# Optimization experiments

Hardware: AMD Instinct MI355X
Metric: run time of the kernel (lower is better)

Reference implementation:

```python
import jax, jax.numpy as jnp
import numpy as np

B, N, D, E, R = 2, 50000, 128, 500000, 500
LN_EPS = 1e-5


def setup_inputs() -> dict:
    key = jax.random.key(0)
    ks = jax.random.split(key, 12)
    s = 1.0 / np.sqrt(D)
    s2 = 1.0 / np.sqrt(2 * D)
    return {
        "h": jax.random.normal(ks[0], (B, N, D), dtype=jnp.float32),
        "edge_src": jax.random.randint(ks[1], (E,), 0, N),
        "edge_tgt": jax.random.randint(ks[2], (E,), 0, N),
        "edge_rel": jax.random.randint(ks[3], (E,), 0, R),
        "nE": N,
        "msg_W": jax.random.uniform(ks[4], (D, D), jnp.float32, -s, s),
        "rel_emb": jax.random.normal(ks[5], (R, D), dtype=jnp.float32),
        "gate_W": jax.random.uniform(ks[6], (D, D), jnp.float32, -s, s),
        "update_W": jax.random.uniform(ks[7], (2 * D, D), jnp.float32, -s2, s2),
        "update_b": jax.random.uniform(ks[8], (D,), jnp.float32, -s2, s2),
        "ln_gamma": jnp.ones((D,), jnp.float32),
        "ln_beta": jnp.zeros((D,), jnp.float32),
    }


def reference(h, edge_src, edge_tgt, edge_rel, nE, msg_W, rel_emb, gate_W,
              update_W, update_b, ln_gamma, ln_beta):
    r = rel_emb[edge_rel]                      # [E, D]
    h_src = h[:, edge_src]                     # [B, E, D] gather
    gate = jax.nn.sigmoid(h_src @ gate_W)      # [B, E, D]
    msg = (h_src @ msg_W) * r[None] * gate     # [B, E, D]
    # scatter_add over target nodes
    h_agg = jnp.zeros((h.shape[0], nE, h.shape[2]), h.dtype)
    h_agg = h_agg.at[:, edge_tgt].add(msg)     # [B, N, D]
    upd = jnp.concatenate([h, h_agg], axis=-1) @ update_W + update_b
    x = h + jax.nn.relu(upd)
    mu = jnp.mean(x, axis=-1, keepdims=True)
    var = jnp.var(x, axis=-1, keepdims=True)
    h_new = (x - mu) * jax.lax.rsqrt(var + LN_EPS) * ln_gamma + ln_beta
    return h_new
```

## Files before the change

### kernel.cpp

```cpp
#include <hip/hip_runtime.h>

#define DD 128
#define NN 50000
#define BB 2
#define EE 500000
#define CAP 64
#define LN_EPS 1e-5f

typedef __attribute__((ext_vector_type(8))) short bf16x8;
typedef __attribute__((ext_vector_type(4))) float f32x4;

union FragU { unsigned short u[8]; unsigned int q[4]; bf16x8 v; };

__device__ __forceinline__ unsigned short f2bf(float x) {
  union { float f; unsigned u; } v; v.f = x;
  unsigned r = (v.u + 0x7FFFu + ((v.u >> 16) & 1u)) >> 16;
  return (unsigned short)r;
}
__device__ __forceinline__ float bfbits(short s) {
  union { unsigned u; float f; } v;
  v.u = ((unsigned)(unsigned short)s) << 16;
  return v.f;
}
__device__ __forceinline__ float sigmoidf(float x) {
  return 1.0f / (1.0f + __expf(-x));
}

__device__ __forceinline__ void stage16(const void* g, void* l) {
  __builtin_amdgcn_global_load_lds(
      (const __attribute__((address_space(1))) unsigned int*)g,
      (__attribute__((address_space(3))) unsigned int*)l, 16, 0, 0);
}

__global__ __launch_bounds__(256) void k_node(
    const float* __restrict__ h, const float* __restrict__ gate_W,
    const float* __restrict__ msg_W, unsigned short* __restrict__ P,
    int* __restrict__ deg, int BN)
{
  __shared__ float Hs[3][2048];

  const int t    = threadIdx.x;

  {
    const int gid  = blockIdx.x * 256 + t;
    const int gsz2 = gridDim.x * 256;
    for (int i = gid; i < NN; i += gsz2) deg[i] = 0;
    asm volatile("s_waitcnt vmcnt(0)" ::: "memory");
    __builtin_amdgcn_sched_barrier(0);
  }

  const int lane = t & 63;
  const int n16  = lane & 15;
  const int quad = lane >> 4;
  const int wave = t >> 6;

  FragU ag[2][4], am[2][4];
#pragma unroll
  for (int fi = 0; fi < 2; fi++) {
    const int frow = (wave + fi * 4) * 16 + n16;
#pragma unroll
    for (int ks = 0; ks < 4; ks++) {
      const int k0 = ks * 32 + quad * 8;
#pragma unroll
      for (int e = 0; e < 8; e++) {
        ag[fi][ks].u[e] = f2bf(gate_W[(size_t)(k0 + e) * DD + frow]);
        am[fi][ks].u[e] = f2bf(msg_W[(size_t)(k0 + e) * DD + frow]);
      }
    }
  }

  const int sr = t >> 5, sc = t & 31;
  const size_t g0 = (size_t)sr * 512 +
                    (size_t)((((sc & 24) | ((sc & 7) ^ (sr & 7)))) << 4);

  const int nT    = BN >> 4;
  const int gstep = gridDim.x;
  const int bid   = blockIdx.x;
  const char* hB  = (const char*)h;

#define NSTAGE(slot, tl)                                                     \
  do {                                                                       \
    const char* gb = hB + ((size_t)(tl) << 13);                              \
    char* lb = (char*)&Hs[slot][0];                                          \
    stage16(gb + g0, lb + t * 16);                                           \
    stage16(gb + g0 + 4096, lb + 4096 + t * 16);                             \
  } while (0)

  if (bid < nT)         NSTAGE(0, bid);
  if (bid + gstep < nT) NSTAGE(1, bid + gstep);

  int s = 0;
  for (int tile = bid; tile < nT; tile += gstep) {
    asm volatile("s_waitcnt vmcnt(2)" ::: "memory");
    __builtin_amdgcn_s_barrier();
    asm volatile("" ::: "memory");
    __builtin_amdgcn_sched_barrier(0);

    const float* hs = &Hs[s][0];
    bf16x8 bfr[4];
#pragma unroll
    for (int ks = 0; ks < 4; ks++) {
      const int cc = ks * 8 + quad * 2;
      const int w0 = (cc & 24) | ((cc & 7) ^ (n16 & 7));
      const int w1 = ((cc + 1) & 24) | (((cc + 1) & 7) ^ (n16 & 7));
      const float4 x0 = *(const float4*)(hs + n16 * 128 + w0 * 4);
      const float4 x1 = *(const float4*)(hs + n16 * 128 + w1 * 4);
      FragU f;
      f.u[0] = f2bf(x0.x); f.u[1] = f2bf(x0.y);
      f.u[2] = f2bf(x0.z); f.u[3] = f2bf(x0.w);
      f.u[4] = f2bf(x1.x); f.u[5] = f2bf(x1.y);
      f.u[6] = f2bf(x1.z); f.u[7] = f2bf(x1.w);
      bfr[ks] = f.v;
    }

    f32x4 accg[2], accm[2];
#pragma unroll
    for (int fi = 0; fi < 2; fi++) { accg[fi] = (f32x4)0.f; accm[fi] = (f32x4)0.f; }

#pragma unroll
    for (int fi = 0; fi < 2; fi++)
#pragma unroll
      for (int ks = 0; ks < 4; ks++) {
        accg[fi] = __builtin_amdgcn_mfma_f32_16x16x32_bf16(ag[fi][ks].v, bfr[ks], accg[fi], 0, 0, 0);
        accm[fi] = __builtin_amdgcn_mfma_f32_16x16x32_bf16(am[fi][ks].v, bfr[ks], accm[fi], 0, 0, 0);
      }

    const int b    = (tile * 16 >= NN) ? 1 : 0;
    const int node = tile * 16 + n16 - b * NN;
    unsigned short* Pr = P + (size_t)node * 256 + b * 128;
#pragma unroll
    for (int fi = 0; fi < 2; fi++) {
      const int ft = wave + fi * 4;
      const float v0 = accm[fi][0] * sigmoidf(accg[fi][0]);
      const float v1 = accm[fi][1] * sigmoidf(accg[fi][1]);
      const float v2 = accm[fi][2] * sigmoidf(accg[fi][2]);
      const float v3 = accm[fi][3] * sigmoidf(accg[fi][3]);
      uint2 o;
      o.x = (unsigned int)f2bf(v0) | ((unsigned int)f2bf(v1) << 16);
      o.y = (unsigned int)f2bf(v2) | ((unsigned int)f2bf(v3) << 16);
      *(uint2*)(Pr + ft * 16 + quad * 4) = o;
    }

    asm volatile("" ::: "memory");
    if (tile + 2 * gstep < nT) {
      int s2 = s + 2; if (s2 >= 3) s2 -= 3;
      NSTAGE(s2, tile + 2 * gstep);
    }
    s = (s + 1 >= 3) ? 0 : s + 1;
  }
#undef NSTAGE
}

__global__ __launch_bounds__(256) void k_fill_direct(
    const int* __restrict__ esrc, const int* __restrict__ etgt,
    const int* __restrict__ erel, int* __restrict__ deg,
    int* __restrict__ packed)
{
  const int e = blockIdx.x * 256 + threadIdx.x;
  if (e < EE) {
    const int tgt = etgt[e];
    const int pos = atomicAdd(&deg[tgt], 1);
    if (pos < CAP) packed[(size_t)tgt * CAP + pos] = esrc[e] | (erel[e] << 16);
  }
}

__global__ __launch_bounds__(256) void k_agg(
    const unsigned short* __restrict__ P, const float* __restrict__ rel_emb,
    const int* __restrict__ deg, const int* __restrict__ packed,
    unsigned short* __restrict__ h_agg)
{
  const int node = blockIdx.x * 4 + (threadIdx.x >> 6);
  if (node >= NN) return;
  const int lane = threadIdx.x & 63;
  const int half = lane >> 5;
  const int c8   = (lane & 31) * 8;
  const int rc   = c8 & 127;

  const int beg = node * CAP;
  const int cnt = min(deg[node], CAP);
  const int end = beg + cnt;

  float acc[8];
#pragma unroll
  for (int i = 0; i < 8; i++) acc[i] = 0.f;

  int j = beg + half;
  for (; j + 2 < end; j += 4) {
    const int p0 = packed[j];
    const int p1 = packed[j + 2];
    const bf16x8 pv0 = *(const bf16x8*)(P + (size_t)(p0 & 0xFFFF) * 256 + c8);
    const float4 ra0 = *(const float4*)(rel_emb + (size_t)(p0 >> 16) * DD + rc);
    const float4 rb0 = *(const float4*)(rel_emb + (size_t)(p0 >> 16) * DD + rc + 4);
    const bf16x8 pv1 = *(const bf16x8*)(P + (size_t)(p1 & 0xFFFF) * 256 + c8);
    const float4 ra1 = *(const float4*)(rel_emb + (size_t)(p1 >> 16) * DD + rc);
    const float4 rb1 = *(const float4*)(rel_emb + (size_t)(p1 >> 16) * DD + rc + 4);
    acc[0] += bfbits(pv0[0]) * ra0.x;  acc[0] += bfbits(pv1[0]) * ra1.x;
    acc[1] += bfbits(pv0[1]) * ra0.y;  acc[1] += bfbits(pv1[1]) * ra1.y;
    acc[2] += bfbits(pv0[2]) * ra0.z;  acc[2] += bfbits(pv1[2]) * ra1.z;
    acc[3] += bfbits(pv0[3]) * ra0.w;  acc[3] += bfbits(pv1[3]) * ra1.w;
    acc[4] += bfbits(pv0[4]) * rb0.x;  acc[4] += bfbits(pv1[4]) * rb1.x;
    acc[5] += bfbits(pv0[5]) * rb0.y;  acc[5] += bfbits(pv1[5]) * rb1.y;
    acc[6] += bfbits(pv0[6]) * rb0.z;  acc[6] += bfbits(pv1[6]) * rb1.z;
    acc[7] += bfbits(pv0[7]) * rb0.w;  acc[7] += bfbits(pv1[7]) * rb1.w;
  }
  for (; j < end; j += 2) {
    const int p0 = packed[j];
    const bf16x8 pv0 = *(const bf16x8*)(P + (size_t)(p0 & 0xFFFF) * 256 + c8);
    const float4 ra0 = *(const float4*)(rel_emb + (size_t)(p0 >> 16) * DD + rc);
    const float4 rb0 = *(const float4*)(rel_emb + (size_t)(p0 >> 16) * DD + rc + 4);
    acc[0] += bfbits(pv0[0]) * ra0.x;
    acc[1] += bfbits(pv0[1]) * ra0.y;
    acc[2] += bfbits(pv0[2]) * ra0.z;
    acc[3] += bfbits(pv0[3]) * ra0.w;
    acc[4] += bfbits(pv0[4]) * rb0.x;
    acc[5] += bfbits(pv0[5]) * rb0.y;
    acc[6] += bfbits(pv0[6]) * rb0.z;
    acc[7] += bfbits(pv0[7]) * rb0.w;
  }

#pragma unroll
  for (int i = 0; i < 8; i++) acc[i] += __shfl_xor(acc[i], 32, 64);

  if (half == 0) {
    uint4 o;
    o.x = (unsigned int)f2bf(acc[0]) | ((unsigned int)f2bf(acc[1]) << 16);
    o.y = (unsigned int)f2bf(acc[2]) | ((unsigned int)f2bf(acc[3]) << 16);
    o.z = (unsigned int)f2bf(acc[4]) | ((unsigned int)f2bf(acc[5]) << 16);
    o.w = (unsigned int)f2bf(acc[6]) | ((unsigned int)f2bf(acc[7]) << 16);
    *(uint4*)(h_agg + (size_t)node * 256 + c8) = o;
  }
}

__global__ __launch_bounds__(256) void k_update_ln(
    const float* __restrict__ h, const unsigned short* __restrict__ h_agg,
    const float* __restrict__ upd_W, const float* __restrict__ upd_b,
    const float* __restrict__ gamma, const float* __restrict__ beta,
    float* __restrict__ out, int BN)
{
  __shared__ float Us[3][3072];
  __shared__ float Rs[4][16], Rq[4][16];

  const int t    = threadIdx.x;
  const int lane = t & 63;
  const int n16  = lane & 15;
  const int quad = lane >> 4;
  const int wave = t >> 6;

  FragU aw[2][8];
#pragma unroll
  for (int fi = 0; fi < 2; fi++) {
    const int frow = (wave + fi * 4) * 16 + n16;
#pragma unroll
    for (int ks = 0; ks < 8; ks++) {
      const int k0 = ks * 32 + quad * 8;
#pragma unroll
      for (int e = 0; e < 8; e++)
        aw[fi][ks].u[e] = f2bf(upd_W[(size_t)(k0 + e) * DD + frow]);
    }
  }

  float4 bv[2], gv[2], btv[2];
#pragma unroll
  for (int fi = 0; fi < 2; fi++) {
    const int f0 = (wave + fi * 4) * 16 + quad * 4;
    bv[fi]  = *(const float4*)(upd_b + f0);
    gv[fi]  = *(const float4*)(gamma + f0);
    btv[fi] = *(const float4*)(beta + f0);
  }

  const int sr = t >> 5, sc = t & 31;
  const size_t g0 = (size_t)sr * 512 +
                    (size_t)((((sc & 24) | ((sc & 7) ^ (sr & 7)))) << 4);
  const int ar = t >> 4, ac = t & 15;
  const size_t ga0 = (size_t)ar * 512 +
                     (size_t)((((ac & 8) | ((ac & 7) ^ (ar & 7)))) << 4);

  const int nT    = BN >> 4;
  const int gstep = gridDim.x;
  const int bid   = blockIdx.x;
  const char* hB  = (const char*)h;
  const char* aB  = (const char*)h_agg;

#define USTAGE(slot, tl)                                                     \
  do {                                                                       \
    const char* gb = hB + ((size_t)(tl) << 13);                              \
    char* lb = (char*)&Us[slot][0];                                          \
    stage16(gb + g0, lb + t * 16);                                           \
    stage16(gb + g0 + 4096, lb + 4096 + t * 16);                             \
    const int bb = ((tl) * 16 >= NN) ? 1 : 0;                                \
    const size_t node0 = (size_t)(tl) * 16 - (size_t)bb * NN;                \
    stage16(aB + (node0 << 9) + ((size_t)bb << 8) + ga0, lb + 8192 + t * 16);\
  } while (0)

  if (bid < nT)         USTAGE(0, bid);
  if (bid + gstep < nT) USTAGE(1, bid + gstep);

  int s = 0;
  for (int tile = bid; tile < nT; tile += gstep) {
    asm volatile("s_waitcnt vmcnt(3)" ::: "memory");
    __builtin_amdgcn_s_barrier();
    asm volatile("" ::: "memory");
    __builtin_amdgcn_sched_barrier(0);

    const float* hs = &Us[s][0];
    const unsigned short* ha = (const unsigned short*)(hs + 2048);

    bf16x8 bfr[8];
#pragma unroll
    for (int ks = 0; ks < 4; ks++) {
      const int cc = ks * 8 + quad * 2;
      const int w0 = (cc & 24) | ((cc & 7) ^ (n16 & 7));
      const int w1 = ((cc + 1) & 24) | (((cc + 1) & 7) ^ (n16 & 7));
      const float4 x0 = *(const float4*)(hs + n16 * 128 + w0 * 4);
      const float4 x1 = *(const float4*)(hs + n16 * 128 + w1 * 4);
      FragU f;
      f.u[0] = f2bf(x0.x); f.u[1] = f2bf(x0.y);
      f.u[2] = f2bf(x0.z); f.u[3] = f2bf(x0.w);
      f.u[4] = f2bf(x1.x); f.u[5] = f2bf(x1.y);
      f.u[6] = f2bf(x1.z); f.u[7] = f2bf(x1.w);
      bfr[ks] = f.v;
    }
#pragma unroll
    for (int ks = 0; ks < 4; ks++) {
      const int c  = ks * 4 + quad;
      const int wc = (c & 8) | ((c & 7) ^ (n16 & 7));
      bfr[4 + ks] = *(const bf16x8*)(ha + n16 * 128 + wc * 8);
    }

    f32x4 acc[2];
#pragma unroll
    for (int fi = 0; fi < 2; fi++) acc[fi] = (f32x4)0.f;
#pragma unroll
    for (int fi = 0; fi < 2; fi++)
#pragma unroll
      for (int ks = 0; ks < 8; ks++)
        acc[fi] = __builtin_amdgcn_mfma_f32_16x16x32_bf16(aw[fi][ks].v, bfr[ks], acc[fi], 0, 0, 0);

    float xv[2][4];
    float p1 = 0.f, p2 = 0.f;
#pragma unroll
    for (int fi = 0; fi < 2; fi++) {
      const int ft = wave + fi * 4;
      const int cr = ft * 4 + quad;
      const int wr = (cr & 24) | ((cr & 7) ^ (n16 & 7));
      const float4 hv = *(const float4*)(hs + n16 * 128 + wr * 4);
      xv[fi][0] = hv.x + fmaxf(acc[fi][0] + bv[fi].x, 0.f);
      xv[fi][1] = hv.y + fmaxf(acc[fi][1] + bv[fi].y, 0.f);
      xv[fi][2] = hv.z + fmaxf(acc[fi][2] + bv[fi].z, 0.f);
      xv[fi][3] = hv.w + fmaxf(acc[fi][3] + bv[fi].w, 0.f);
#pragma unroll
      for (int r = 0; r < 4; r++) { p1 += xv[fi][r]; p2 += xv[fi][r] * xv[fi][r]; }
    }
    p1 += __shfl_xor(p1, 16, 64); p2 += __shfl_xor(p2, 16, 64);
    p1 += __shfl_xor(p1, 32, 64); p2 += __shfl_xor(p2, 32, 64);
    if (quad == 0) { Rs[wave][n16] = p1; Rq[wave][n16] = p2; }
    asm volatile("s_waitcnt lgkmcnt(0)" ::: "memory");
    __builtin_amdgcn_s_barrier();
    asm volatile("" ::: "memory");
    const float sA = Rs[0][n16] + Rs[1][n16] + Rs[2][n16] + Rs[3][n16];
    const float sB = Rq[0][n16] + Rq[1][n16] + Rq[2][n16] + Rq[3][n16];

    const float mu   = sA * (1.0f / DD);
    const float var  = sB * (1.0f / DD) - mu * mu;
    const float rstd = rsqrtf(var + LN_EPS);

    const size_t nrow = (size_t)tile * 16 + n16;
#pragma unroll
    for (int fi = 0; fi < 2; fi++) {
      const int f0 = (wave + fi * 4) * 16 + quad * 4;
      float4 o;
      o.x = (xv[fi][0] - mu) * rstd * gv[fi].x + btv[fi].x;
      o.y = (xv[fi][1] - mu) * rstd * gv[fi].y + btv[fi].y;
      o.z = (xv[fi][2] - mu) * rstd * gv[fi].z + btv[fi].z;
      o.w = (xv[fi][3] - mu) * rstd * gv[fi].w + btv[fi].w;
      *(float4*)(out + nrow * DD + f0) = o;
    }

    asm volatile("" ::: "memory");
    if (tile + 2 * gstep < nT) {
      int s2 = s + 2; if (s2 >= 3) s2 -= 3;
      USTAGE(s2, tile + 2 * gstep);
    }
    s = (s + 1 >= 3) ? 0 : s + 1;
  }
#undef USTAGE
}

extern "C" void kernel_launch(void* const* d_in, const int* in_sizes, int n_in,
                              void* d_out, int out_size, void* d_ws, size_t ws_size,
                              hipStream_t stream) {
  const float* h       = (const float*)d_in[0];
  const int*   esrc    = (const int*)d_in[1];
  const int*   etgt    = (const int*)d_in[2];
  const int*   erel    = (const int*)d_in[3];
  const float* msg_W   = (const float*)d_in[5];
  const float* rel_emb = (const float*)d_in[6];
  const float* gate_W  = (const float*)d_in[7];
  const float* upd_W   = (const float*)d_in[8];
  const float* upd_b   = (const float*)d_in[9];
  const float* gamma   = (const float*)d_in[10];
  const float* beta    = (const float*)d_in[11];
  float*       out     = (float*)d_out;

  const int BN = in_sizes[0] / DD;

  unsigned short* P     = (unsigned short*)d_ws;
  unsigned short* h_agg = P + (size_t)NN * 256;
  int* deg    = (int*)(h_agg + (size_t)NN * 256);
  int* packed = deg + NN;

  const int nbE = (EE + 255) / 256;

  k_node<<<512, 256, 0, stream>>>(h, gate_W, msg_W, P, deg, BN);

  k_fill_direct<<<nbE, 256, 0, stream>>>(esrc, etgt, erel, deg, packed);

  k_agg<<<(NN + 3) / 4, 256, 0, stream>>>(P, rel_emb, deg, packed, h_agg);

  k_update_ln<<<512, 256, 0, stream>>>(h, h_agg, upd_W, upd_b,
                                       gamma, beta, out, BN);
}
```

Baseline: 227.2 us.

## Fuse edge aggregation into update+LayerNorm kernel, keep h_agg in shared memory

```diff
diff --git a/kernel.cpp b/kernel.cpp
--- a/kernel.cpp
+++ b/kernel.cpp
@@ -164,87 +164,25 @@
   }
 }
 
-__global__ __launch_bounds__(256) void k_agg(
-    const unsigned short* __restrict__ P, const float* __restrict__ rel_emb,
-    const int* __restrict__ deg, const int* __restrict__ packed,
-    unsigned short* __restrict__ h_agg)
+__global__ __launch_bounds__(256) void k_upd(
+    const float* __restrict__ h, const unsigned short* __restrict__ P,
+    const float* __restrict__ rel_emb, const int* __restrict__ deg,
+    const int* __restrict__ packed, const float* __restrict__ upd_W,
+    const float* __restrict__ upd_b, const float* __restrict__ gamma,
+    const float* __restrict__ beta, float* __restrict__ out)
 {
-  const int node = blockIdx.x * 4 + (threadIdx.x >> 6);
-  if (node >= NN) return;
-  const int lane = threadIdx.x & 63;
-  const int half = lane >> 5;
-  const int c8   = (lane & 31) * 8;
-  const int rc   = c8 & 127;
-
-  const int beg = node * CAP;
-  const int cnt = min(deg[node], CAP);
-  const int end = beg + cnt;
-
-  float acc[8];
-#pragma unroll
-  for (int i = 0; i < 8; i++) acc[i] = 0.f;
-
-  int j = beg + half;
-  for (; j + 2 < end; j += 4) {
-    const int p0 = packed[j];
-    const int p1 = packed[j + 2];
-    const bf16x8 pv0 = *(const bf16x8*)(P + (size_t)(p0 & 0xFFFF) * 256 + c8);
-    const float4 ra0 = *(const float4*)(rel_emb + (size_t)(p0 >> 16) * DD + rc);
-    const float4 rb0 = *(const float4*)(rel_emb + (size_t)(p0 >> 16) * DD + rc + 4);
-    const bf16x8 pv1 = *(const bf16x8*)(P + (size_t)(p1 & 0xFFFF) * 256 + c8);
-    const float4 ra1 = *(const float4*)(rel_emb + (size_t)(p1 >> 16) * DD + rc);
-    const float4 rb1 = *(const float4*)(rel_emb + (size_t)(p1 >> 16) * DD + rc + 4);
-    acc[0] += bfbits(pv0[0]) * ra0.x;  acc[0] += bfbits(pv1[0]) * ra1.x;
-    acc[1] += bfbits(pv0[1]) * ra0.y;  acc[1] += bfbits(pv1[1]) * ra1.y;
-    acc[2] += bfbits(pv0[2]) * ra0.z;  acc[2] += bfbits(pv1[2]) * ra1.z;
-    acc[3] += bfbits(pv0[3]) * ra0.w;  acc[3] += bfbits(pv1[3]) * ra1.w;
-    acc[4] += bfbits(pv0[4]) * rb0.x;  acc[4] += bfbits(pv1[4]) * rb1.x;
-    acc[5] += bfbits(pv0[5]) * rb0.y;  acc[5] += bfbits(pv1[5]) * rb1.y;
-    acc[6] += bfbits(pv0[6]) * rb0.z;  acc[6] += bfbits(pv1[6]) * rb1.z;
-    acc[7] += bfbits(pv0[7]) * rb0.w;  acc[7] += bfbits(pv1[7]) * rb1.w;
-  }
-  for (; j < end; j += 2) {
-    const int p0 = packed[j];
-    const bf16x8 pv0 = *(const bf16x8*)(P + (size_t)(p0 & 0xFFFF) * 256 + c8);
-    const float4 ra0 = *(const float4*)(rel_emb + (size_t)(p0 >> 16) * DD + rc);
-    const float4 rb0 = *(const float4*)(rel_emb + (size_t)(p0 >> 16) * DD + rc + 4);
-    acc[0] += bfbits(pv0[0]) * ra0.x;
-    acc[1] += bfbits(pv0[1]) * ra0.y;
-    acc[2] += bfbits(pv0[2]) * ra0.z;
-    acc[3] += bfbits(pv0[3]) * ra0.w;
-    acc[4] += bfbits(pv0[4]) * rb0.x;
-    acc[5] += bfbits(pv0[5]) * rb0.y;
-    acc[6] += bfbits(pv0[6]) * rb0.z;
-    acc[7] += bfbits(pv0[7]) * rb0.w;
-  }
-
-#pragma unroll
-  for (int i = 0; i < 8; i++) acc[i] += __shfl_xor(acc[i], 32, 64);
-
-  if (half == 0) {
-    uint4 o;
-    o.x = (unsigned int)f2bf(acc[0]) | ((unsigned int)f2bf(acc[1]) << 16);
-    o.y = (unsigned int)f2bf(acc[2]) | ((unsigned int)f2bf(acc[3]) << 16);
-    o.z = (unsigned int)f2bf(acc[4]) | ((unsigned int)f2bf(acc[5]) << 16);
-    o.w = (unsigned int)f2bf(acc[6]) | ((unsigned int)f2bf(acc[7]) << 16);
-    *(uint4*)(h_agg + (size_t)node * 256 + c8) = o;
-  }
-}
-
-__global__ __launch_bounds__(256) void k_update_ln(
-    const float* __restrict__ h, const unsigned short* __restrict__ h_agg,
-    const float* __restrict__ upd_W, const float* __restrict__ upd_b,
-    const float* __restrict__ gamma, const float* __restrict__ beta,
-    float* __restrict__ out, int BN)
-{
-  __shared__ float Us[3][3072];
-  __shared__ float Rs[4][16], Rq[4][16];
+  __shared__ unsigned short Ab[16 * 256];
+  __shared__ float Hb[2 * 2048];
+  __shared__ float Rs[2][4][16], Rq[2][4][16];
 
   const int t    = threadIdx.x;
   const int lane = t & 63;
   const int n16  = lane & 15;
   const int quad = lane >> 4;
   const int wave = t >> 6;
+  const int half = lane >> 5;
+  const int c8   = (lane & 31) * 8;
+  const int rc   = c8 & 127;
 
   FragU aw[2][8];
 #pragma unroll
@@ -268,122 +206,167 @@
     btv[fi] = *(const float4*)(beta + f0);
   }
 
-  const int sr = t >> 5, sc = t & 31;
-  const size_t g0 = (size_t)sr * 512 +
-                    (size_t)((((sc & 24) | ((sc & 7) ^ (sr & 7)))) << 4);
-  const int ar = t >> 4, ac = t & 15;
-  const size_t ga0 = (size_t)ar * 512 +
-                     (size_t)((((ac & 8) | ((ac & 7) ^ (ar & 7)))) << 4);
-
-  const int nT    = BN >> 4;
+  const int sr  = t >> 5, sc = t & 31;
+  const int scw  = (sc & 24) | ((sc & 7) ^ (sr & 7));
+  const int scw2 = (sc & 24) | ((sc & 7) ^ ((sr + 8) & 7));
+
+  const int nTL   = NN / 16;
   const int gstep = gridDim.x;
   const int bid   = blockIdx.x;
-  const char* hB  = (const char*)h;
-  const char* aB  = (const char*)h_agg;
-
-#define USTAGE(slot, tl)                                                     \
-  do {                                                                       \
-    const char* gb = hB + ((size_t)(tl) << 13);                              \
-    char* lb = (char*)&Us[slot][0];                                          \
-    stage16(gb + g0, lb + t * 16);                                           \
-    stage16(gb + g0 + 4096, lb + 4096 + t * 16);                             \
-    const int bb = ((tl) * 16 >= NN) ? 1 : 0;                                \
-    const size_t node0 = (size_t)(tl) * 16 - (size_t)bb * NN;                \
-    stage16(aB + (node0 << 9) + ((size_t)bb << 8) + ga0, lb + 8192 + t * 16);\
-  } while (0)
-
-  if (bid < nT)         USTAGE(0, bid);
-  if (bid + gstep < nT) USTAGE(1, bid + gstep);
-
-  int s = 0;
-  for (int tile = bid; tile < nT; tile += gstep) {
-    asm volatile("s_waitcnt vmcnt(3)" ::: "memory");
-    __builtin_amdgcn_s_barrier();
-    asm volatile("" ::: "memory");
-    __builtin_amdgcn_sched_barrier(0);
-
-    const float* hs = &Us[s][0];
-    const unsigned short* ha = (const unsigned short*)(hs + 2048);
-
-    bf16x8 bfr[8];
-#pragma unroll
-    for (int ks = 0; ks < 4; ks++) {
-      const int cc = ks * 8 + quad * 2;
-      const int w0 = (cc & 24) | ((cc & 7) ^ (n16 & 7));
-      const int w1 = ((cc + 1) & 24) | (((cc + 1) & 7) ^ (n16 & 7));
-      const float4 x0 = *(const float4*)(hs + n16 * 128 + w0 * 4);
-      const float4 x1 = *(const float4*)(hs + n16 * 128 + w1 * 4);
-      FragU f;
-      f.u[0] = f2bf(x0.x); f.u[1] = f2bf(x0.y);
-      f.u[2] = f2bf(x0.z); f.u[3] = f2bf(x0.w);
-      f.u[4] = f2bf(x1.x); f.u[5] = f2bf(x1.y);
-      f.u[6] = f2bf(x1.z); f.u[7] = f2bf(x1.w);
-      bfr[ks] = f.v;
-    }
-#pragma unroll
-    for (int ks = 0; ks < 4; ks++) {
-      const int c  = ks * 4 + quad;
-      const int wc = (c & 8) | ((c & 7) ^ (n16 & 7));
-      bfr[4 + ks] = *(const bf16x8*)(ha + n16 * 128 + wc * 8);
-    }
-
-    f32x4 acc[2];
-#pragma unroll
-    for (int fi = 0; fi < 2; fi++) acc[fi] = (f32x4)0.f;
-#pragma unroll
-    for (int fi = 0; fi < 2; fi++)
-#pragma unroll
-      for (int ks = 0; ks < 8; ks++)
-        acc[fi] = __builtin_amdgcn_mfma_f32_16x16x32_bf16(aw[fi][ks].v, bfr[ks], acc[fi], 0, 0, 0);
-
-    float xv[2][4];
-    float p1 = 0.f, p2 = 0.f;
-#pragma unroll
-    for (int fi = 0; fi < 2; fi++) {
-      const int ft = wave + fi * 4;
-      const int cr = ft * 4 + quad;
-      const int wr = (cr & 24) | ((cr & 7) ^ (n16 & 7));
-      const float4 hv = *(const float4*)(hs + n16 * 128 + wr * 4);
-      xv[fi][0] = hv.x + fmaxf(acc[fi][0] + bv[fi].x, 0.f);
-      xv[fi][1] = hv.y + fmaxf(acc[fi][1] + bv[fi].y, 0.f);
-      xv[fi][2] = hv.z + fmaxf(acc[fi][2] + bv[fi].z, 0.f);
-      xv[fi][3] = hv.w + fmaxf(acc[fi][3] + bv[fi].w, 0.f);
-#pragma unroll
-      for (int r = 0; r < 4; r++) { p1 += xv[fi][r]; p2 += xv[fi][r] * xv[fi][r]; }
-    }
-    p1 += __shfl_xor(p1, 16, 64); p2 += __shfl_xor(p2, 16, 64);
-    p1 += __shfl_xor(p1, 32, 64); p2 += __shfl_xor(p2, 32, 64);
-    if (quad == 0) { Rs[wave][n16] = p1; Rq[wave][n16] = p2; }
+
+  for (int tl = bid; tl < nTL; tl += gstep) {
+    {
+      const size_t r0 = (size_t)tl * 16;
+      const float4 ha0 = *(const float4*)(h + (r0 + sr) * DD + sc * 4);
+      const float4 ha1 = *(const float4*)(h + (r0 + sr + 8) * DD + sc * 4);
+      const float4 hb0 = *(const float4*)(h + (r0 + NN + sr) * DD + sc * 4);
+      const float4 hb1 = *(const float4*)(h + (r0 + NN + sr + 8) * DD + sc * 4);
+
+      for (int rr = 0; rr < 4; rr++) {
+        const int r = wave * 4 + rr;
+        const int n = tl * 16 + r;
+        const int beg = n * CAP;
+        const int dg  = deg[n];
+        const int end = beg + (dg < CAP ? dg : CAP);
+        float acc[8];
+#pragma unroll
+        for (int i = 0; i < 8; i++) acc[i] = 0.f;
+        int j = beg + half;
+        for (; j + 2 < end; j += 4) {
+          const int p0 = packed[j];
+          const int p1 = packed[j + 2];
+          const bf16x8 pv0 = *(const bf16x8*)(P + (size_t)(p0 & 0xFFFF) * 256 + c8);
+          const float4 ra0 = *(const float4*)(rel_emb + (size_t)(p0 >> 16) * DD + rc);
+          const float4 rb0 = *(const float4*)(rel_emb + (size_t)(p0 >> 16) * DD + rc + 4);
+          const bf16x8 pv1 = *(const bf16x8*)(P + (size_t)(p1 & 0xFFFF) * 256 + c8);
+          const float4 ra1 = *(const float4*)(rel_emb + (size_t)(p1 >> 16) * DD + rc);
+          const float4 rb1 = *(const float4*)(rel_emb + (size_t)(p1 >> 16) * DD + rc + 4);
+          acc[0] += bfbits(pv0[0]) * ra0.x;  acc[0] += bfbits(pv1[0]) * ra1.x;
+          acc[1] += bfbits(pv0[1]) * ra0.y;  acc[1] += bfbits(pv1[1]) * ra1.y;
+          acc[2] += bfbits(pv0[2]) * ra0.z;  acc[2] += bfbits(pv1[2]) * ra1.z;
+          acc[3] += bfbits(pv0[3]) * ra0.w;  acc[3] += bfbits(pv1[3]) * ra1.w;
+          acc[4] += bfbits(pv0[4]) * rb0.x;  acc[4] += bfbits(pv1[4]) * rb1.x;
+          acc[5] += bfbits(pv0[5]) * rb0.y;  acc[5] += bfbits(pv1[5]) * rb1.y;
+          acc[6] += bfbits(pv0[6]) * rb0.z;  acc[6] += bfbits(pv1[6]) * rb1.z;
+          acc[7] += bfbits(pv0[7]) * rb0.w;  acc[7] += bfbits(pv1[7]) * rb1.w;
+        }
+        for (; j < end; j += 2) {
+          const int p0 = packed[j];
+          const bf16x8 pv0 = *(const bf16x8*)(P + (size_t)(p0 & 0xFFFF) * 256 + c8);
+          const float4 ra0 = *(const float4*)(rel_emb + (size_t)(p0 >> 16) * DD + rc);
+          const float4 rb0 = *(const float4*)(rel_emb + (size_t)(p0 >> 16) * DD + rc + 4);
+          acc[0] += bfbits(pv0[0]) * ra0.x;
+          acc[1] += bfbits(pv0[1]) * ra0.y;
+          acc[2] += bfbits(pv0[2]) * ra0.z;
+          acc[3] += bfbits(pv0[3]) * ra0.w;
+          acc[4] += bfbits(pv0[4]) * rb0.x;
+          acc[5] += bfbits(pv0[5]) * rb0.y;
+          acc[6] += bfbits(pv0[6]) * rb0.z;
+          acc[7] += bfbits(pv0[7]) * rb0.w;
+        }
+#pragma unroll
+        for (int i = 0; i < 8; i++) acc[i] += __shfl_xor(acc[i], 32, 64);
+        if (half == 0) {
+          uint4 o;
+          o.x = (unsigned int)f2bf(acc[0]) | ((unsigned int)f2bf(acc[1]) << 16);
+          o.y = (unsigned int)f2bf(acc[2]) | ((unsigned int)f2bf(acc[3]) << 16);
+          o.z = (unsigned int)f2bf(acc[4]) | ((unsigned int)f2bf(acc[5]) << 16);
+          o.w = (unsigned int)f2bf(acc[6]) | ((unsigned int)f2bf(acc[7]) << 16);
+          const int g   = lane;
+          const int gsw = (g & 24) | ((g & 7) ^ (r & 7));
+          *(uint4*)&Ab[r * 256 + gsw * 8] = o;
+        }
+      }
+      *(float4*)&Hb[0 * 2048 + sr * 128 + scw * 4]        = ha0;
+      *(float4*)&Hb[0 * 2048 + (sr + 8) * 128 + scw2 * 4] = ha1;
+      *(float4*)&Hb[1 * 2048 + sr * 128 + scw * 4]        = hb0;
+      *(float4*)&Hb[1 * 2048 + (sr + 8) * 128 + scw2 * 4] = hb1;
+    }
     asm volatile("s_waitcnt lgkmcnt(0)" ::: "memory");
     __builtin_amdgcn_s_barrier();
     asm volatile("" ::: "memory");
-    const float sA = Rs[0][n16] + Rs[1][n16] + Rs[2][n16] + Rs[3][n16];
-    const float sB = Rq[0][n16] + Rq[1][n16] + Rq[2][n16] + Rq[3][n16];
-
-    const float mu   = sA * (1.0f / DD);
-    const float var  = sB * (1.0f / DD) - mu * mu;
-    const float rstd = rsqrtf(var + LN_EPS);
-
-    const size_t nrow = (size_t)tile * 16 + n16;
-#pragma unroll
-    for (int fi = 0; fi < 2; fi++) {
-      const int f0 = (wave + fi * 4) * 16 + quad * 4;
-      float4 o;
-      o.x = (xv[fi][0] - mu) * rstd * gv[fi].x + btv[fi].x;
-      o.y = (xv[fi][1] - mu) * rstd * gv[fi].y + btv[fi].y;
-      o.z = (xv[fi][2] - mu) * rstd * gv[fi].z + btv[fi].z;
-      o.w = (xv[fi][3] - mu) * rstd * gv[fi].w + btv[fi].w;
-      *(float4*)(out + nrow * DD + f0) = o;
-    }
-
+
+#pragma unroll
+    for (int tau = 0; tau < 2; tau++) {
+      const float* hs = &Hb[tau * 2048];
+      const unsigned short* ab = &Ab[0];
+
+      bf16x8 bfr[8];
+#pragma unroll
+      for (int ks = 0; ks < 4; ks++) {
+        const int cc = ks * 8 + quad * 2;
+        const int w0 = (cc & 24) | ((cc & 7) ^ (n16 & 7));
+        const int w1 = ((cc + 1) & 24) | (((cc + 1) & 7) ^ (n16 & 7));
+        const float4 x0 = *(const float4*)(hs + n16 * 128 + w0 * 4);
+        const float4 x1 = *(const float4*)(hs + n16 * 128 + w1 * 4);
+        FragU f;
+        f.u[0] = f2bf(x0.x); f.u[1] = f2bf(x0.y);
+        f.u[2] = f2bf(x0.z); f.u[3] = f2bf(x0.w);
+        f.u[4] = f2bf(x1.x); f.u[5] = f2bf(x1.y);
+        f.u[6] = f2bf(x1.z); f.u[7] = f2bf(x1.w);
+        bfr[ks] = f.v;
+      }
+#pragma unroll
+      for (int ks = 0; ks < 4; ks++) {
+        const int g   = tau * 16 + ks * 4 + quad;
+        const int gsw = (g & 24) | ((g & 7) ^ (n16 & 7));
+        bfr[4 + ks] = *(const bf16x8*)(ab + n16 * 256 + gsw * 8);
+      }
+
+      f32x4 acc2[2];
+#pragma unroll
+      for (int fi = 0; fi < 2; fi++) acc2[fi] = (f32x4)0.f;
+#pragma unroll
+      for (int fi = 0; fi < 2; fi++)
+#pragma unroll
+        for (int ks = 0; ks < 8; ks++)
+          acc2[fi] = __builtin_amdgcn_mfma_f32_16x16x32_bf16(aw[fi][ks].v, bfr[ks], acc2[fi], 0, 0, 0);
+
+      float xv[2][4];
+      float p1 = 0.f, p2 = 0.f;
+#pragma unroll
+      for (int fi = 0; fi < 2; fi++) {
+        const int ft = wave + fi * 4;
+        const int cr = ft * 4 + quad;
+        const int wr = (cr & 24) | ((cr & 7) ^ (n16 & 7));
+        const float4 hv = *(const float4*)(hs + n16 * 128 + wr * 4);
+        xv[fi][0] = hv.x + fmaxf(acc2[fi][0] + bv[fi].x, 0.f);
+        xv[fi][1] = hv.y + fmaxf(acc2[fi][1] + bv[fi].y, 0.f);
+        xv[fi][2] = hv.z + fmaxf(acc2[fi][2] + bv[fi].z, 0.f);
+        xv[fi][3] = hv.w + fmaxf(acc2[fi][3] + bv[fi].w, 0.f);
+#pragma unroll
+        for (int r = 0; r < 4; r++) { p1 += xv[fi][r]; p2 += xv[fi][r] * xv[fi][r]; }
+      }
+      p1 += __shfl_xor(p1, 16, 64); p2 += __shfl_xor(p2, 16, 64);
+      p1 += __shfl_xor(p1, 32, 64); p2 += __shfl_xor(p2, 32, 64);
+      if (quad == 0) { Rs[tau][wave][n16] = p1; Rq[tau][wave][n16] = p2; }
+      asm volatile("s_waitcnt lgkmcnt(0)" ::: "memory");
+      __builtin_amdgcn_s_barrier();
+      asm volatile("" ::: "memory");
+      const float sA = Rs[tau][0][n16] + Rs[tau][1][n16] + Rs[tau][2][n16] + Rs[tau][3][n16];
+      const float sB = Rq[tau][0][n16] + Rq[tau][1][n16] + Rq[tau][2][n16] + Rq[tau][3][n16];
+
+      const float mu   = sA * (1.0f / DD);
+      const float var  = sB * (1.0f / DD) - mu * mu;
+      const float rstd = rsqrtf(var + LN_EPS);
+
+      const size_t nrow = (size_t)tau * NN + (size_t)tl * 16 + n16;
+#pragma unroll
+      for (int fi = 0; fi < 2; fi++) {
+        const int f0 = (wave + fi * 4) * 16 + quad * 4;
+        float4 o;
+        o.x = (xv[fi][0] - mu) * rstd * gv[fi].x + btv[fi].x;
+        o.y = (xv[fi][1] - mu) * rstd * gv[fi].y + btv[fi].y;
+        o.z = (xv[fi][2] - mu) * rstd * gv[fi].z + btv[fi].z;
+        o.w = (xv[fi][3] - mu) * rstd * gv[fi].w + btv[fi].w;
+        *(float4*)(out + nrow * DD + f0) = o;
+      }
+    }
+
+    asm volatile("s_waitcnt lgkmcnt(0)" ::: "memory");
+    __builtin_amdgcn_s_barrier();
     asm volatile("" ::: "memory");
-    if (tile + 2 * gstep < nT) {
-      int s2 = s + 2; if (s2 >= 3) s2 -= 3;
-      USTAGE(s2, tile + 2 * gstep);
-    }
-    s = (s + 1 >= 3) ? 0 : s + 1;
-  }
-#undef USTAGE
+  }
 }
 
 extern "C" void kernel_launch(void* const* d_in, const int* in_sizes, int n_in,
@@ -404,9 +387,8 @@
 
   const int BN = in_sizes[0] / DD;
 
-  unsigned short* P     = (unsigned short*)d_ws;
-  unsigned short* h_agg = P + (size_t)NN * 256;
-  int* deg    = (int*)(h_agg + (size_t)NN * 256);
+  unsigned short* P = (unsigned short*)d_ws;
+  int* deg    = (int*)(P + (size_t)NN * 256);
   int* packed = deg + NN;
 
   const int nbE = (EE + 255) / 256;
@@ -415,8 +397,6 @@
 
   k_fill_direct<<<nbE, 256, 0, stream>>>(esrc, etgt, erel, deg, packed);
 
-  k_agg<<<(NN + 3) / 4, 256, 0, stream>>>(P, rel_emb, deg, packed, h_agg);
-
-  k_update_ln<<<512, 256, 0, stream>>>(h, h_agg, upd_W, upd_b,
-                                       gamma, beta, out, BN);
-}
+  k_upd<<<1024, 256, 0, stream>>>(h, P, rel_emb, deg, packed, upd_W, upd_b,
+                                  gamma, beta, out);
+}
```

New measurement: 274.0 us. +20.6%, slower.
